# Optimization experiments

Measured on AMD Instinct MI355X. Metric: run time of the kernel, lower is better.

The kernel has to match this reference:

```python
import jax, jax.numpy as jnp
import numpy as np

LMBD = 0.1      # cfg['MODEL']['LAMBDA'][0]
MU = 0.1        # ISTA/FISTA step size (cfg['MODEL']['MU'])
N_STEPS = 4     # cfg['MODEL']['NUM_LAYERS']
FISTA = True    # cfg['MODEL']['ISFISTA']


def _conv(x, W, s, p):
    # torch F.conv2d, NCHW / OIHW
    return jax.lax.conv_general_dilated(x, W, (s, s), [(p, p), (p, p)],
        dimension_numbers=('NCHW', 'OIHW', 'NCHW'))


def _conv_t(z, W, s, p):
    # torch F.conv_transpose2d(z, W, stride=s, padding=p): output (H-1)*s + k - 2p
    k = W.shape[-1]
    Wt = jnp.transpose(jnp.flip(W, (-2, -1)), (1, 0, 2, 3))
    pad = k - 1 - p
    return jax.lax.conv_general_dilated(z, Wt, (1, 1), [(pad, pad), (pad, pad)],
        lhs_dilation=(s, s), dimension_numbers=('NCHW', 'OIHW', 'NCHW'))


def _wnorm(W):
    # per-atom unit-norm dictionary (w_norm=True)
    return W / (jnp.sqrt(jnp.sum(W * W, axis=(1, 2, 3), keepdims=True)) + 1e-12)


def _dict_block(x, W, s, p):
    # unrolled FISTA sparse coding: min_z 0.5||x - W^T*z||^2 + lmbd||z||_1, z>=0
    thr = MU * LMBD
    shrink = lambda u: jax.nn.relu(u - thr)  # non-negative soft threshold
    z0 = shrink(MU * _conv(x, W, s, p))

    def body(carry, _):
        z, z_old, t = carry
        if FISTA:
            t_new = (1.0 + jnp.sqrt(1.0 + 4.0 * t * t)) * 0.5
            y = z + ((t - 1.0) / t_new) * (z - z_old)
        else:
            t_new, y = t, z
        r = x - _conv_t(y, W, s, p)                 # residual in image space
        z_new = shrink(y + MU * _conv(r, W, s, p))  # gradient step + shrinkage
        return (z_new, z, t_new), None

    (z, _, _), _ = jax.lax.scan(body, (z0, z0, jnp.float32(1.0)), None, length=N_STEPS - 1)
    return z


def _bn(x, eps=1e-5):
    # BatchNorm2d at init (gamma=1, beta=0), training-mode batch stats, biased var
    m = jnp.mean(x, axis=(0, 2, 3), keepdims=True)
    v = jnp.var(x, axis=(0, 2, 3), keepdims=True)
    return (x - m) * jax.lax.rsqrt(v + eps)


def _lrelu(x):
    return jnp.where(x >= 0, x, 0.2 * x)


def setup_inputs() -> dict:
    key = jax.random.key(0)
    ks = jax.random.split(key, 7)
    nc, ndf, nz = 3, 64, 128

    def kaiming(k, shape):
        fan_in = shape[1] * shape[2] * shape[3]
        bound = float(np.sqrt(6.0 / fan_in))
        return jax.random.uniform(k, shape, jnp.float32, -bound, bound)

    return {
        'x':  jax.random.normal(ks[0], (64, nc, 96, 96), jnp.float32),
        'W1': kaiming(ks[1], (ndf, nc, 4, 4)),
        'W2': kaiming(ks[2], (ndf * 2, ndf, 4, 4)),
        'W3': kaiming(ks[3], (ndf * 4, ndf * 2, 4, 4)),
        'W4': kaiming(ks[4], (ndf * 8, ndf * 4, 4, 4)),
        'W5': kaiming(ks[5], (ndf * 16, ndf * 8, 4, 4)),
        'W6': kaiming(ks[6], (nz, ndf * 16, 3, 3)),
    }


def reference(x, W1, W2, W3, W4, W5, W6):
    Ws = [_wnorm(w) for w in (W1, W2, W3, W4, W5, W6)]
    # encoder: 96 -> 48 -> 24 -> 12 -> 6 -> 3 -> 1
    o = _lrelu(_dict_block(x, Ws[0], 2, 1))
    for i in range(1, 5):
        o = _lrelu(_bn(_dict_block(o, Ws[i], 2, 1)))
    z = _dict_block(o, Ws[5], 1, 0).reshape(x.shape[0], -1)
    z = z / jnp.maximum(jnp.linalg.norm(z, axis=1, keepdims=True), 1e-12)  # F.normalize
    # decoder (DictConv2d.inverse chain, uses the normalized dictionaries)
    h = z.reshape(z.shape[0], -1, 1, 1)
    h = jax.nn.relu(_bn(_conv_t(h, Ws[5], 1, 0)))
    for i in (4, 3, 2, 1):
        h = jax.nn.relu(_bn(_conv_t(h, Ws[i], 2, 1)))
    x_hat = jnp.tanh(_conv_t(h, Ws[0], 2, 1))
    return z, x_hat
```

## Files before the change

kernel.cpp:

```cpp
#include <hip/hip_runtime.h>
#include <math.h>

#define BLK 256
static constexpr float MU_F  = 0.1f;
static constexpr float THR_F = 0.01f;

typedef __attribute__((ext_vector_type(8))) short bf16x8;
typedef __attribute__((ext_vector_type(4))) float f32x4;

__device__ inline unsigned short f2bf(float f) {
    unsigned u = __float_as_uint(f);
    unsigned r = (u + 0x7fffu + ((u >> 16) & 1u)) >> 16;
    return (unsigned short)r;
}
__device__ inline float bf2f(unsigned short h) {
    return __uint_as_float(((unsigned)h) << 16);
}

__device__ inline float blk_reduce(float v) {
    __shared__ float sh[BLK];
    int tid = threadIdx.x;
    sh[tid] = v;
    __syncthreads();
    #pragma unroll
    for (int s = BLK / 2; s > 0; s >>= 1) {
        if (tid < s) sh[tid] += sh[tid + s];
        __syncthreads();
    }
    float r = sh[0];
    __syncthreads();
    return r;
}

__global__ __launch_bounds__(BLK) void wnorm_pack(
    const float* __restrict__ W, float* __restrict__ Wkc,
    float* __restrict__ Wnout, int Mout, int asz)
{
    int o = blockIdx.x;
    const float* w = W + (size_t)o * asz;
    float s = 0.f;
    for (int i = threadIdx.x; i < asz; i += BLK) { float v = w[i]; s = fmaf(v, v, s); }
    float tot = blk_reduce(s);
    float inv = 1.0f / (sqrtf(tot) + 1e-12f);
    for (int i = threadIdx.x; i < asz; i += BLK) {
        float v = w[i] * inv;
        Wkc[(size_t)i * Mout + o] = v;
        if (Wnout) Wnout[(size_t)o * asz + i] = v;
    }
}

__global__ __launch_bounds__(BLK) void wnorm_pack_bf16(
    const float* __restrict__ W, short* __restrict__ Cpk, short* __restrict__ Tpk,
    int Cout, int Cin)
{
    int o = blockIdx.x;
    int asz = Cin * 16;
    const float* w = W + (size_t)o * asz;
    float s = 0.f;
    for (int i = threadIdx.x; i < asz; i += BLK) { float v = w[i]; s = fmaf(v, v, s); }
    float tot = blk_reduce(s);
    float inv = 1.0f / (sqrtf(tot) + 1e-12f);
    size_t cTot = (size_t)Cout * asz;
    size_t parStride = (size_t)Cout * 4 * Cin;
    size_t tTot = 4 * parStride;
    for (int i = threadIdx.x; i < asz; i += BLK) {
        float v = w[i] * inv;
        unsigned short hb = f2bf(v);
        unsigned short lb = f2bf(v - bf2f(hb));
        size_t cidx = ((size_t)(i >> 3)) * (Cout * 8) + o * 8 + (i & 7);
        Cpk[cidx] = (short)hb;
        Cpk[cTot + cidx] = (short)lb;
        int c = i >> 4, tap = i & 15, kh = tap >> 2, kw = tap & 3;
        int par = (1 - (kh & 1)) * 2 + (1 - (kw & 1));
        int tt = ((kh >> 1) << 1) | (kw >> 1);
        int q = o * 4 + tt;
        size_t tidx = (size_t)par * parStride + ((size_t)(q >> 3)) * (Cin * 8) + c * 8 + (q & 7);
        Tpk[tidx] = (short)hb;
        Tpk[tTot + tidx] = (short)lb;
    }
}

__device__ inline void xcd_remap(int& bx, int& by, int& bz) {
    int nx = gridDim.x, ny = gridDim.y;
    int nwg = nx * ny * gridDim.z;
    int orig = blockIdx.x + nx * (blockIdx.y + ny * blockIdx.z);
    int q8 = nwg >> 3, r8 = nwg & 7, xcd = orig & 7, sidx = orig >> 3;
    int w = (xcd < r8 ? xcd * (q8 + 1) : r8 * (q8 + 1) + (xcd - r8) * q8) + sidx;
    bx = w % nx; int t = w / nx; by = t % ny; bz = t / ny;
}

__global__ __launch_bounds__(BLK) void conv_gemm_bf16(
    const short* __restrict__ Wpk, const float* __restrict__ x,
    const float* __restrict__ yin, float* __restrict__ out,
    int M, int Cx, int Hx, int Wx, int Hout, int Wout,
    int kchunk, int emode)
{
    __shared__ __align__(16) short Wh[4][64][8];
    __shared__ __align__(16) short Wo_[4][64][8];
    __shared__ __align__(16) short Xh[4][64][8];
    __shared__ __align__(16) short Xo[4][64][8];
    int bx, by, bz; xcd_remap(bx, by, bz);
    int tid = threadIdx.x, lane = tid & 63, wid = tid >> 6;
    int HW = Hout * Wout, HWx = Hx * Wx;
    int pbase = bx * 64, m0 = by * 64, kb = bz * kchunk;
    size_t loOff = (size_t)Cx * 16 * M;

    int spl = tid & 63, skb = tid >> 6;
    int sp = pbase + spl;
    int sn = sp / HW; int srr = sp - sn * HW;
    int sho = srr / Wout, swo = srr - sho * Wout;
    const float* xs = x + (size_t)sn * Cx * HWx;
    int h0 = sho * 2 - 1, w0 = swo * 2 - 1;

    int t16 = (skb & 1) * 8;
    int offs[8]; bool valt[8];
    #pragma unroll
    for (int jj = 0; jj < 8; ++jj) {
        int tap = t16 + jj;
        int kh = tap >> 2, kw = tap & 3;
        int h = h0 + kh, w = w0 + kw;
        valt[jj] = ((unsigned)h < (unsigned)Hx) && ((unsigned)w < (unsigned)Wx);
        offs[jj] = h * Wx + w;
    }
    const float* xc = xs + ((size_t)(kb >> 4) + (skb >> 1)) * HWx;

    f32x4 acc[4] = {};
    for (int k0 = kb; k0 < kb + kchunk; k0 += 32) {
        size_t so = ((size_t)((k0 >> 3) + skb)) * (M * 8) + (size_t)m0 * 8 + spl * 8;
        *(float4*)(&Wh[skb][spl][0])  = *(const float4*)(Wpk + so);
        *(float4*)(&Wo_[skb][spl][0]) = *(const float4*)(Wpk + loOff + so);
        {
            union { short s[8]; float4 f; } uh, ul;
            #pragma unroll
            for (int jj = 0; jj < 8; ++jj) {
                float g = valt[jj] ? xc[offs[jj]] : 0.f;
                unsigned short hb = (unsigned short)(__float_as_uint(g) >> 16);
                uh.s[jj] = (short)hb;
                ul.s[jj] = (short)f2bf(g - bf2f(hb));
            }
            *(float4*)(&Xh[skb][spl][0]) = uh.f;
            *(float4*)(&Xo[skb][spl][0]) = ul.f;
        }
        xc += 2 * HWx;
        __syncthreads();
        bf16x8 ah = *(const bf16x8*)(&Wh[lane >> 4][wid * 16 + (lane & 15)][0]);
        bf16x8 al = *(const bf16x8*)(&Wo_[lane >> 4][wid * 16 + (lane & 15)][0]);
        #pragma unroll
        for (int nf = 0; nf < 4; ++nf) {
            bf16x8 bh = *(const bf16x8*)(&Xh[lane >> 4][nf * 16 + (lane & 15)][0]);
            bf16x8 bl = *(const bf16x8*)(&Xo[lane >> 4][nf * 16 + (lane & 15)][0]);
            acc[nf] = __builtin_amdgcn_mfma_f32_16x16x32_bf16(al, bh, acc[nf], 0, 0, 0);
            acc[nf] = __builtin_amdgcn_mfma_f32_16x16x32_bf16(ah, bl, acc[nf], 0, 0, 0);
            acc[nf] = __builtin_amdgcn_mfma_f32_16x16x32_bf16(ah, bh, acc[nf], 0, 0, 0);
        }
        __syncthreads();
    }
    int colp = lane & 15, rquad = lane >> 4;
    #pragma unroll
    for (int nf = 0; nf < 4; ++nf) {
        int p = pbase + nf * 16 + colp;
        int n = p / HW; int rr = p - n * HW;
        int ho = rr / Wout, wo = rr - ho * Wout;
        #pragma unroll
        for (int r = 0; r < 4; ++r) {
            int m = m0 + wid * 16 + rquad * 4 + r;
            size_t idx = (((size_t)n * M + m) * Hout + ho) * Wout + wo;
            float v = acc[nf][r];
            if (emode == 0)      out[idx] = fmaxf(MU_F * v - THR_F, 0.f);
            else if (emode == 1) out[idx] = fmaxf(yin[idx] + MU_F * v - THR_F, 0.f);
            else                 atomicAdd(&out[idx], v);
        }
    }
}

__global__ __launch_bounds__(BLK) void convt_gemm_bf16(
    const short* __restrict__ Wpk, const float* __restrict__ z,
    const float* __restrict__ aux, float* __restrict__ out,
    int M, int Cz, int Hz, int Wz, int Ho, int Wo, int emode, int SK)
{
    __shared__ __align__(16) short Wh[4][64][8];
    __shared__ __align__(16) short Wo_[4][64][8];
    __shared__ __align__(16) short Xh[4][64][8];
    __shared__ __align__(16) short Xo[4][64][8];
    int bx, by, bz; xcd_remap(bx, by, bz);
    int tid = threadIdx.x, lane = tid & 63, wid = tid >> 6;
    int par = bz / SK, chunk = bz - par * SK;
    int hbit = par >> 1, wbit = par & 1;
    int czs = Cz / SK;
    int qb = chunk * czs * 4;
    size_t parS = (size_t)Cz * 4 * M;
    const short* Wp = Wpk + (size_t)par * parS;
    size_t loOff = 4 * parS;
    int Hc = Ho >> 1, Wc = Wo >> 1, HWc = Hc * Wc;
    int pbase = bx * 64, m0 = by * 64;

    int spl = tid & 63, skb = tid >> 6;
    int sp = pbase + spl;
    int sn = sp / HWc; int srr = sp - sn * HWc;
    int shc = srr / Wc, swc = srr - shc * Wc;
    int HWz = Hz * Wz;
    const float* zs = z + (size_t)sn * Cz * HWz;

    int offt[4]; bool valt[4];
    #pragma unroll
    for (int t = 0; t < 4; ++t) {
        int ti = t >> 1, tj = t & 1;
        int hn = shc + hbit - ti, wn = swc + wbit - tj;
        valt[t] = ((unsigned)hn < (unsigned)Hz) && ((unsigned)wn < (unsigned)Wz);
        offt[t] = hn * Wz + wn;
    }
    const float* zc = zs + ((size_t)(qb >> 2) + skb * 2) * HWz;

    f32x4 acc[4] = {};
    for (int q0 = qb; q0 < qb + czs * 4; q0 += 32) {
        size_t so = ((size_t)((q0 >> 3) + skb)) * (M * 8) + (size_t)m0 * 8 + spl * 8;
        *(float4*)(&Wh[skb][spl][0])  = *(const float4*)(Wp + so);
        *(float4*)(&Wo_[skb][spl][0]) = *(const float4*)(Wp + loOff + so);
        {
            union { short s[8]; float4 f; } uh, ul;
            #pragma unroll
            for (int jj = 0; jj < 8; ++jj) {
                int t = jj & 3;
                float g = valt[t] ? zc[(jj >> 2) * HWz + offt[t]] : 0.f;
                unsigned short hb = (unsigned short)(__float_as_uint(g) >> 16);
                uh.s[jj] = (short)hb;
                ul.s[jj] = (short)f2bf(g - bf2f(hb));
            }
            *(float4*)(&Xh[skb][spl][0]) = uh.f;
            *(float4*)(&Xo[skb][spl][0]) = ul.f;
        }
        zc += 8 * HWz;
        __syncthreads();
        bf16x8 ah = *(const bf16x8*)(&Wh[lane >> 4][wid * 16 + (lane & 15)][0]);
        bf16x8 al = *(const bf16x8*)(&Wo_[lane >> 4][wid * 16 + (lane & 15)][0]);
        #pragma unroll
        for (int nf = 0; nf < 4; ++nf) {
            bf16x8 bh = *(const bf16x8*)(&Xh[lane >> 4][nf * 16 + (lane & 15)][0]);
            bf16x8 bl = *(const bf16x8*)(&Xo[lane >> 4][nf * 16 + (lane & 15)][0]);
            acc[nf] = __builtin_amdgcn_mfma_f32_16x16x32_bf16(al, bh, acc[nf], 0, 0, 0);
            acc[nf] = __builtin_amdgcn_mfma_f32_16x16x32_bf16(ah, bl, acc[nf], 0, 0, 0);
            acc[nf] = __builtin_amdgcn_mfma_f32_16x16x32_bf16(ah, bh, acc[nf], 0, 0, 0);
        }
        __syncthreads();
    }
    int colp = lane & 15, rquad = lane >> 4;
    #pragma unroll
    for (int nf = 0; nf < 4; ++nf) {
        int p = pbase + nf * 16 + colp;
        int n = p / HWc; int rr = p - n * HWc;
        int hc = rr / Wc, wc = rr - hc * Wc;
        int ho = 2 * hc + hbit, wo = 2 * wc + wbit;
        #pragma unroll
        for (int r = 0; r < 4; ++r) {
            int m = m0 + wid * 16 + rquad * 4 + r;
            size_t idx = (((size_t)n * M + m) * Ho + ho) * Wo + wo;
            float v = acc[nf][r];
            if (emode == 0)      out[idx] = aux[idx] - v;
            else if (emode == 1) out[idx] = v;
            else                 atomicAdd(&out[idx], v);
        }
    }
}

template <int KK, int Kk, int S, int P>
__global__ __launch_bounds__(BLK) void conv_gemm(
    const float* __restrict__ Wp, const float* __restrict__ x,
    const float* __restrict__ yin, float* __restrict__ out,
    int M, int Ktot, int Cx, int Hx, int Wx, int Hout, int Wout,
    int kchunk, int emode)
{
    __shared__ float Wt[16][64];
    __shared__ float Xt[16][64];
    int tid = threadIdx.x, tx = tid & 15, ty = tid >> 4;
    int HW = Hout * Wout, HWx = Hx * Wx;
    int pbase = blockIdx.x * 64 + tx * 4;
    int n_[4], ho_[4], wo_[4];
    const float* xb_[4];
    #pragma unroll
    for (int j = 0; j < 4; ++j) {
        int p = pbase + j; int n = p / HW; int r = p - n * HW;
        int ho = r / Wout; int wo = r - ho * Wout;
        n_[j] = n; ho_[j] = ho; wo_[j] = wo;
        xb_[j] = x + (size_t)n * Cx * HWx;
    }
    int m0 = blockIdx.y * 64;
    int kb = blockIdx.z * kchunk, ke = kb + kchunk;
    if (ke > Ktot) ke = Ktot;
    float acc[4][4] = {};
    for (int k0 = kb; k0 < ke; k0 += 16) {
        int kr = k0 + ty;
        *(float4*)&Wt[ty][tx * 4] = *(const float4*)&Wp[(size_t)kr * M + m0 + tx * 4];
        int ci = kr / KK; int t = kr - ci * KK; int kh = t / Kk; int kw = t - kh * Kk;
        int cio = ci * HWx;
        float g[4];
        #pragma unroll
        for (int j = 0; j < 4; ++j) {
            int h = ho_[j] * S - P + kh, w = wo_[j] * S - P + kw;
            g[j] = ((unsigned)h < (unsigned)Hx && (unsigned)w < (unsigned)Wx)
                 ? xb_[j][cio + h * Wx + w] : 0.f;
        }
        *(float4*)&Xt[ty][tx * 4] = make_float4(g[0], g[1], g[2], g[3]);
        __syncthreads();
        #pragma unroll
        for (int kk = 0; kk < 16; ++kk) {
            float4 a = *(float4*)&Wt[kk][ty * 4];
            float4 b = *(float4*)&Xt[kk][tx * 4];
            float aa[4] = {a.x, a.y, a.z, a.w};
            float bb[4] = {b.x, b.y, b.z, b.w};
            #pragma unroll
            for (int i = 0; i < 4; ++i)
                #pragma unroll
                for (int j = 0; j < 4; ++j)
                    acc[i][j] = fmaf(aa[i], bb[j], acc[i][j]);
        }
        __syncthreads();
    }
    #pragma unroll
    for (int i = 0; i < 4; ++i) {
        int m = m0 + ty * 4 + i;
        #pragma unroll
        for (int j = 0; j < 4; ++j) {
            size_t idx = (((size_t)n_[j] * M + m) * Hout + ho_[j]) * Wout + wo_[j];
            float v = acc[i][j];
            if (emode == 0)      out[idx] = fmaxf(MU_F * v - THR_F, 0.f);
            else if (emode == 1) out[idx] = fmaxf(yin[idx] + MU_F * v - THR_F, 0.f);
            else                 atomicAdd(&out[idx], v);
        }
    }
}

__global__ __launch_bounds__(BLK) void outer_gemm(
    const float* __restrict__ Wp, const float* __restrict__ zin,
    const float* __restrict__ aux, float* __restrict__ out,
    int M, int Kz, int emode)
{
    __shared__ float Wt[16][64];
    __shared__ float Xt[16][64];
    int tid = threadIdx.x, tx = tid & 15, ty = tid >> 4;
    int m0 = blockIdx.y * 64;
    float acc[4][4] = {};
    for (int k0 = 0; k0 < Kz; k0 += 16) {
        int kr = k0 + ty;
        *(float4*)&Wt[ty][tx * 4] = *(const float4*)&Wp[(size_t)kr * M + m0 + tx * 4];
        float g[4];
        #pragma unroll
        for (int j = 0; j < 4; ++j) g[j] = zin[(size_t)(tx * 4 + j) * Kz + kr];
        *(float4*)&Xt[ty][tx * 4] = make_float4(g[0], g[1], g[2], g[3]);
        __syncthreads();
        #pragma unroll
        for (int kk = 0; kk < 16; ++kk) {
            float4 a = *(float4*)&Wt[kk][ty * 4];
            float4 b = *(float4*)&Xt[kk][tx * 4];
            float aa[4] = {a.x, a.y, a.z, a.w};
            float bb[4] = {b.x, b.y, b.z, b.w};
            #pragma unroll
            for (int i = 0; i < 4; ++i)
                #pragma unroll
                for (int j = 0; j < 4; ++j)
                    acc[i][j] = fmaf(aa[i], bb[j], acc[i][j]);
        }
        __syncthreads();
    }
    #pragma unroll
    for (int i = 0; i < 4; ++i) {
        int m = m0 + ty * 4 + i;
        #pragma unroll
        for (int j = 0; j < 4; ++j) {
            int n = tx * 4 + j;
            size_t idx = (size_t)n * M + m;
            float v = acc[i][j];
            out[idx] = (emode == 0) ? (aux[idx] - v) : v;
        }
    }
}

__global__ __launch_bounds__(BLK) void convt_m3(
    const float* __restrict__ Wkc0, const float* __restrict__ z,
    const float* __restrict__ aux, float* __restrict__ out,
    int Cz, int Hz, int Wz, int Ho, int Wo, int emode)
{
    __shared__ float Wl[64 * 4 * 3];
    int tid = threadIdx.x;
    int hbit = blockIdx.z >> 1, wbit = blockIdx.z & 1;
    int khp = 1 - hbit, kwp = 1 - wbit;
    int Ktot = Cz * 4;
    for (int kidx = tid; kidx < Ktot; kidx += BLK) {
        int cz = kidx >> 2, t = kidx & 3, ti = t >> 1, tj = t & 1;
        int tap = (khp + 2 * ti) * 4 + (kwp + 2 * tj);
        Wl[kidx * 3 + 0] = Wkc0[(0 * 16 + tap) * 64 + cz];
        Wl[kidx * 3 + 1] = Wkc0[(1 * 16 + tap) * 64 + cz];
        Wl[kidx * 3 + 2] = Wkc0[(2 * 16 + tap) * 64 + cz];
    }
    __syncthreads();
    int Hc = Ho >> 1, Wc = Wo >> 1, HWc = Hc * Wc;
    int p = blockIdx.x * BLK + tid;
    int n = p / HWc, r = p - n * HWc, hc = r / Wc, wc = r - (r / Wc) * Wc;
    const float* zb = z + (size_t)n * Cz * Hz * Wz;
    int offs[4]; bool val[4];
    #pragma unroll
    for (int t = 0; t < 4; ++t) {
        int ti = t >> 1, tj = t & 1;
        int hn = hc + hbit - ti, wn = wc + wbit - tj;
        val[t] = ((unsigned)hn < (unsigned)Hz) && ((unsigned)wn < (unsigned)Wz);
        offs[t] = hn * Wz + wn;
    }
    float a0 = 0.f, a1 = 0.f, a2 = 0.f;
    int HWz = Hz * Wz;
    for (int cz = 0; cz < Cz; ++cz) {
        const float* base = zb + cz * HWz;
        #pragma unroll
        for (int t = 0; t < 4; ++t) {
            float g = val[t] ? base[offs[t]] : 0.f;
            int wi = (cz * 4 + t) * 3;
            a0 = fmaf(g, Wl[wi + 0], a0);
            a1 = fmaf(g, Wl[wi + 1], a1);
            a2 = fmaf(g, Wl[wi + 2], a2);
        }
    }
    int ho = 2 * hc + hbit, wo = 2 * wc + wbit;
    #pragma unroll
    for (int u = 0; u < 3; ++u) {
        float v = (u == 0) ? a0 : (u == 1) ? a1 : a2;
        size_t idx = (((size_t)n * 3 + u) * Ho + ho) * Wo + wo;
        out[idx] = (emode == 0) ? (aux[idx] - v) : tanhf(v);
    }
}

__global__ __launch_bounds__(BLK) void shrink_epi_v4(
    const float* __restrict__ p, const float* __restrict__ y,
    float* __restrict__ o, int n4, int mode)
{
    int i = blockIdx.x * BLK + threadIdx.x;
    if (i >= n4) return;
    float4 pv = ((const float4*)p)[i];
    float4 r;
    if (mode == 1) {
        float4 yv = ((const float4*)y)[i];
        r.x = fmaxf(yv.x + MU_F * pv.x - THR_F, 0.f);
        r.y = fmaxf(yv.y + MU_F * pv.y - THR_F, 0.f);
        r.z = fmaxf(yv.z + MU_F * pv.z - THR_F, 0.f);
        r.w = fmaxf(yv.w + MU_F * pv.w - THR_F, 0.f);
    } else {
        r.x = fmaxf(MU_F * pv.x - THR_F, 0.f);
        r.y = fmaxf(MU_F * pv.y - THR_F, 0.f);
        r.z = fmaxf(MU_F * pv.z - THR_F, 0.f);
        r.w = fmaxf(MU_F * pv.w - THR_F, 0.f);
    }
    ((float4*)o)[i] = r;
}

__global__ __launch_bounds__(BLK) void res_epi_v4(
    const float* __restrict__ aux, const float* __restrict__ acc,
    float* __restrict__ o, int n4)
{
    int i = blockIdx.x * BLK + threadIdx.x;
    if (i >= n4) return;
    float4 a = ((const float4*)aux)[i];
    float4 b = ((const float4*)acc)[i];
    ((float4*)o)[i] = make_float4(a.x - b.x, a.y - b.y, a.z - b.z, a.w - b.w);
}

__global__ __launch_bounds__(BLK) void y_update_v4(
    const float* __restrict__ z, const float* __restrict__ zo,
    float* __restrict__ y, int n4, float c)
{
    int i = blockIdx.x * BLK + threadIdx.x;
    if (i >= n4) return;
    float4 zv = ((const float4*)z)[i];
    float4 ov = ((const float4*)zo)[i];
    ((float4*)y)[i] = make_float4(
        fmaf(c, zv.x - ov.x, zv.x), fmaf(c, zv.y - ov.y, zv.y),
        fmaf(c, zv.z - ov.z, zv.z), fmaf(c, zv.w - ov.w, zv.w));
}

__global__ __launch_bounds__(BLK) void bn_stats_part(
    const float* __restrict__ x, float* __restrict__ stats,
    int N, int C, int HW, int nblk)
{
    int c = blockIdx.x, b = blockIdx.y;
    int cnt = N * HW;
    float s = 0.f, s2 = 0.f;
    for (int i = b * BLK + threadIdx.x; i < cnt; i += nblk * BLK) {
        int n = i / HW, hw = i - n * HW;
        float v = x[((size_t)n * C + c) * HW + hw];
        s += v; s2 = fmaf(v, v, s2);
    }
    float ts  = blk_reduce(s);
    float ts2 = blk_reduce(s2);
    if (threadIdx.x == 0) {
        atomicAdd(&stats[c], ts);
        atomicAdd(&stats[C + c], ts2);
    }
}
__global__ __launch_bounds__(BLK) void bn_finalize(
    const float* __restrict__ stats, float* __restrict__ mean,
    float* __restrict__ rstd, int C, int cnt)
{
    int c = blockIdx.x * BLK + threadIdx.x;
    if (c >= C) return;
    float m = stats[c] / cnt;
    float var = stats[C + c] / cnt - m * m;
    mean[c] = m;
    rstd[c] = rsqrtf(var + 1e-5f);
}

__global__ __launch_bounds__(BLK) void bn_act_v4(
    const float* __restrict__ x, const float* __restrict__ mean,
    const float* __restrict__ rstd, float* __restrict__ out,
    int n4, int C, int HW, int use_bn, int act)
{
    int i = blockIdx.x * BLK + threadIdx.x;
    if (i >= n4) return;
    float4 v = ((const float4*)x)[i];
    float e[4] = {v.x, v.y, v.z, v.w};
    int base = i * 4;
    #pragma unroll
    for (int j = 0; j < 4; ++j) {
        float t = e[j];
        if (use_bn) { int c = ((base + j) / HW) % C; t = (t - mean[c]) * rstd[c]; }
        e[j] = (act == 0) ? ((t >= 0.f) ? t : 0.2f * t) : fmaxf(t, 0.f);
    }
    ((float4*)out)[i] = make_float4(e[0], e[1], e[2], e[3]);
}

__global__ __launch_bounds__(128) void rownorm_kernel(
    const float* __restrict__ z, float* __restrict__ out, float* __restrict__ zvec)
{
    __shared__ float sh[128];
    int r = blockIdx.x, tid = threadIdx.x;
    float v = z[r * 128 + tid];
    sh[tid] = v * v;
    __syncthreads();
    #pragma unroll
    for (int s = 64; s > 0; s >>= 1) {
        if (tid < s) sh[tid] += sh[tid + s];
        __syncthreads();
    }
    float nrm = fmaxf(sqrtf(sh[0]), 1e-12f);
    float o = v / nrm;
    out[r * 128 + tid] = o;
    zvec[r * 128 + tid] = o;
}

static inline int gdiv(int a, int b) { return (a + b - 1) / b; }

extern "C" void kernel_launch(void* const* d_in, const int* in_sizes, int n_in,
                              void* d_out, int out_size, void* d_ws, size_t ws_size,
                              hipStream_t stream)
{
    const float* x = (const float*)d_in[0];
    const float* W[6];
    for (int i = 0; i < 6; ++i) W[i] = (const float*)d_in[1 + i];
    float* ws  = (float*)d_ws;
    float* out = (float*)d_out;

    const int Cin[6]  = {3, 64, 128, 256, 512, 1024};
    const int Cout[6] = {64, 128, 256, 512, 1024, 128};
    const int Hin[6]  = {96, 48, 24, 12, 6, 3};
    const int Hout[6] = {48, 24, 12, 6, 3, 1};
    const int N = 64;
    const int SKc[6] = {1, 1, 2, 4, 8, 1};
    const int SKt[6] = {1, 1, 1, 2, 4, 1};

    size_t off = 0;
    float* Wkc0 = ws + off; off += 3072;
    float* Wkc5 = ws + off; off += 1179648;
    float* Wn5  = ws + off; off += 1179648;
    const size_t csz[5] = {0, 131072, 524288, 2097152, 8388608};
    short* Cpk[5]; short* Tpk[5];
    {
        short* sbase = (short*)(ws + off);
        size_t soff = 0;
        for (int L = 1; L < 5; ++L) { Cpk[L] = sbase + soff; soff += 2 * csz[L]; }
        for (int L = 1; L < 5; ++L) { Tpk[L] = sbase + soff; soff += 2 * csz[L]; }
        off += soff / 2;
    }
    const size_t POOL = 30081024;
    float* pool = ws + off; off += POOL;
    float* xb   = ws + off; off += 9437184;
    float* mean = ws + off; off += 1024;
    float* rstd = ws + off; off += 1024;
    float* stats= ws + off; off += 2048;
    float* zvec = ws + off; off += 8192;
    float* pbuf = ws + off; off += 2359296;

    wnorm_pack<<<64, BLK, 0, stream>>>(W[0], Wkc0, nullptr, 64, 48);
    for (int L = 1; L < 5; ++L)
        wnorm_pack_bf16<<<Cout[L], BLK, 0, stream>>>(W[L], Cpk[L], Tpk[L], Cout[L], Cin[L]);
    wnorm_pack<<<128, BLK, 0, stream>>>(W[5], Wkc5, Wn5, 128, 9216);

    double td = 1.0; float cc[3];
    for (int i = 0; i < 3; ++i) {
        double tn = (1.0 + sqrt(1.0 + 4.0 * td * td)) * 0.5;
        cc[i] = (float)((td - 1.0) / tn);
        td = tn;
    }

    auto run_bn_stats = [&](const float* src, int C, int HW) {
        int cnt = N * HW;
        int nblk = 2048 / C; if (nblk < 1) nblk = 1;
        int maxb = gdiv(cnt, BLK); if (nblk > maxb) nblk = maxb;
        hipMemsetAsync(stats, 0, 2 * C * sizeof(float), stream);
        bn_stats_part<<<dim3(C, nblk), BLK, 0, stream>>>(src, stats, N, C, HW, nblk);
        bn_finalize<<<gdiv(C, BLK), BLK, 0, stream>>>(stats, mean, rstd, C, cnt);
    };

    const float* in = x;
    for (int L = 0; L < 6; ++L) {
        int zTot = N * Cout[L] * Hout[L] * Hout[L];
        int xTot = N * Cin[L] * Hin[L] * Hin[L];
        int npix = N * Hout[L] * Hout[L];
        dim3 ge4(gdiv(zTot / 4, BLK));
        dim3 gr4(gdiv(xTot / 4, BLK));

        float* zA = pool;
        float* zB = pool + (size_t)zTot;
        float* yb = pool + (size_t)2 * zTot;
        float* rb = pool + (size_t)3 * zTot;

        auto launch_conv = [&](const float* src, const float* y, float* dst, int mode) {
            if (L == 5) {
                hipMemsetAsync(pbuf, 0, (size_t)zTot * 4, stream);
                conv_gemm<9, 3, 1, 0><<<dim3(1, 2, 72), BLK, 0, stream>>>(Wkc5, src,
                    nullptr, pbuf, 128, 9216, 1024, 3, 3, 1, 1, 128, 2);
                shrink_epi_v4<<<gdiv(zTot / 4, BLK), BLK, 0, stream>>>(pbuf, y, dst, zTot / 4, mode);
            } else if (L == 0) {
                conv_gemm<16, 4, 2, 1><<<dim3(npix / 64, 1), BLK, 0, stream>>>(
                    Wkc0, src, y, dst, 64, 48, 3, 96, 96, 48, 48, 48, mode);
            } else if (SKc[L] == 1) {
                conv_gemm_bf16<<<dim3(npix / 64, Cout[L] / 64), BLK, 0, stream>>>(
                    Cpk[L], src, y, dst, Cout[L], Cin[L], Hin[L], Hin[L],
                    Hout[L], Hout[L], Cin[L] * 16, mode);
            } else {
                int sk = SKc[L];
                hipMemsetAsync(pbuf, 0, (size_t)zTot * 4, stream);
                conv_gemm_bf16<<<dim3(npix / 64, Cout[L] / 64, sk), BLK, 0, stream>>>(
                    Cpk[L], src, nullptr, pbuf, Cout[L], Cin[L], Hin[L], Hin[L],
                    Hout[L], Hout[L], Cin[L] * 16 / sk, 2);
                shrink_epi_v4<<<gdiv(zTot / 4, BLK), BLK, 0, stream>>>(pbuf, y, dst, zTot / 4, mode);
            }
        };

        launch_conv(in, nullptr, zA, 0);

        float* z = zA; float* zo = zB;
        for (int it = 0; it < 3; ++it) {
            const float* ybp;
            if (it == 0) {
                ybp = z;
            } else {
                y_update_v4<<<ge4, BLK, 0, stream>>>(z, zo, yb, zTot / 4, cc[it]);
                ybp = yb;
            }
            if (L == 0) {
                convt_m3<<<dim3(N * 48 * 48 / BLK, 1, 4), BLK, 0, stream>>>(
                    Wkc0, ybp, in, rb, 64, 48, 48, 96, 96, 0);
            } else if (L < 5) {
                int xpixc = N * (Hin[L] / 2) * (Hin[L] / 2);
                int sk = SKt[L];
                if (sk == 1) {
                    convt_gemm_bf16<<<dim3(xpixc / 64, Cin[L] / 64, 4), BLK, 0, stream>>>(
                        Tpk[L], ybp, in, rb, Cin[L], Cout[L], Hout[L], Hout[L],
                        Hin[L], Hin[L], 0, 1);
                } else {
                    hipMemsetAsync(rb, 0, (size_t)xTot * 4, stream);
                    convt_gemm_bf16<<<dim3(xpixc / 64, Cin[L] / 64, 4 * sk), BLK, 0, stream>>>(
                        Tpk[L], ybp, nullptr, rb, Cin[L], Cout[L], Hout[L], Hout[L],
                        Hin[L], Hin[L], 2, sk);
                    res_epi_v4<<<gr4, BLK, 0, stream>>>(in, rb, rb, xTot / 4);
                }
            } else {
                outer_gemm<<<dim3(1, 144), BLK, 0, stream>>>(Wn5, ybp, in, rb, 9216, 128, 0);
            }
            launch_conv(rb, ybp, zo, 1);
            float* tmp = z; z = zo; zo = tmp;
        }

        int HW = Hout[L] * Hout[L];
        if (L == 0) {
            bn_act_v4<<<ge4, BLK, 0, stream>>>(z, nullptr, nullptr, xb, zTot / 4, Cout[L], HW, 0, 0);
            in = xb;
        } else if (L < 5) {
            run_bn_stats(z, Cout[L], HW);
            bn_act_v4<<<ge4, BLK, 0, stream>>>(z, mean, rstd, xb, zTot / 4, Cout[L], HW, 1, 0);
            in = xb;
        } else {
            rownorm_kernel<<<64, 128, 0, stream>>>(z, out, zvec);
        }
    }

    float* zA = pool;
    float* zB = pool + 9437184;
    {
        int oT = N * 1024 * 9;
        outer_gemm<<<dim3(1, 144), BLK, 0, stream>>>(Wn5, zvec, nullptr, zA, 9216, 128, 1);
        run_bn_stats(zA, 1024, 9);
        bn_act_v4<<<gdiv(oT / 4, BLK), BLK, 0, stream>>>(zA, mean, rstd, zB, oT / 4, 1024, 9, 1, 1);
    }
    float* cur = zB;
    for (int i = 4; i >= 1; --i) {
        int oT = N * Cin[i] * Hin[i] * Hin[i];
        int xpixc = N * (Hin[i] / 2) * (Hin[i] / 2);
        int sk = SKt[i];
        if (sk == 1) {
            convt_gemm_bf16<<<dim3(xpixc / 64, Cin[i] / 64, 4), BLK, 0, stream>>>(
                Tpk[i], cur, nullptr, zA, Cin[i], Cout[i], Hout[i], Hout[i],
                Hin[i], Hin[i], 1, 1);
        } else {
            hipMemsetAsync(zA, 0, (size_t)oT * 4, stream);
            convt_gemm_bf16<<<dim3(xpixc / 64, Cin[i] / 64, 4 * sk), BLK, 0, stream>>>(
                Tpk[i], cur, nullptr, zA, Cin[i], Cout[i], Hout[i], Hout[i],
                Hin[i], Hin[i], 2, sk);
        }
        run_bn_stats(zA, Cin[i], Hin[i] * Hin[i]);
        bn_act_v4<<<gdiv(oT / 4, BLK), BLK, 0, stream>>>(zA, mean, rstd, zB, oT / 4,
            Cin[i], Hin[i] * Hin[i], 1, 1);
        cur = zB;
    }
    convt_m3<<<dim3(N * 48 * 48 / BLK, 1, 4), BLK, 0, stream>>>(
        Wkc0, cur, nullptr, out + 8192, 64, 48, 48, 96, 96, 2);
}
```

Baseline: 3.787 ms.

## Widen bf16 conv GEMM pixel tile to 256 for better weight reuse

Templates the conv and transposed-conv bf16 MFMA GEMM kernels on pixel-tile width. Layers other than layer 4 now use 256-pixel tiles, with each thread gathering one pixel's full 32-wide K slice. Each staged weight tile then feeds four times as many MFMAs, cutting weight traffic and barrier count per flop. The cost is more accumulator registers and LDS per block, plus fewer blocks, which may hurt occupancy and load balance on the smaller layers.

```diff
diff --git a/kernel.cpp b/kernel.cpp
--- a/kernel.cpp
+++ b/kernel.cpp
@@ -89,75 +89,127 @@
     bx = w % nx; int t = w / nx; by = t % ny; bz = t / ny;
 }
 
+template <int PIXB>
 __global__ __launch_bounds__(BLK) void conv_gemm_bf16(
     const short* __restrict__ Wpk, const float* __restrict__ x,
     const float* __restrict__ yin, float* __restrict__ out,
     int M, int Cx, int Hx, int Wx, int Hout, int Wout,
     int kchunk, int emode)
 {
+    constexpr int NF = PIXB / 16;
     __shared__ __align__(16) short Wh[4][64][8];
     __shared__ __align__(16) short Wo_[4][64][8];
-    __shared__ __align__(16) short Xh[4][64][8];
-    __shared__ __align__(16) short Xo[4][64][8];
+    __shared__ __align__(16) short Xh[4][PIXB][8];
+    __shared__ __align__(16) short Xo[4][PIXB][8];
     int bx, by, bz; xcd_remap(bx, by, bz);
     int tid = threadIdx.x, lane = tid & 63, wid = tid >> 6;
     int HW = Hout * Wout, HWx = Hx * Wx;
-    int pbase = bx * 64, m0 = by * 64, kb = bz * kchunk;
+    int pbase = bx * PIXB, m0 = by * 64, kb = bz * kchunk;
     size_t loOff = (size_t)Cx * 16 * M;
-
-    int spl = tid & 63, skb = tid >> 6;
-    int sp = pbase + spl;
+    int wspl = tid & 63, wskb = tid >> 6;
+
+    int sp = pbase + ((PIXB == 64) ? (tid & 63) : tid);
     int sn = sp / HW; int srr = sp - sn * HW;
     int sho = srr / Wout, swo = srr - sho * Wout;
     const float* xs = x + (size_t)sn * Cx * HWx;
     int h0 = sho * 2 - 1, w0 = swo * 2 - 1;
 
-    int t16 = (skb & 1) * 8;
-    int offs[8]; bool valt[8];
-    #pragma unroll
-    for (int jj = 0; jj < 8; ++jj) {
-        int tap = t16 + jj;
-        int kh = tap >> 2, kw = tap & 3;
-        int h = h0 + kh, w = w0 + kw;
-        valt[jj] = ((unsigned)h < (unsigned)Hx) && ((unsigned)w < (unsigned)Wx);
-        offs[jj] = h * Wx + w;
-    }
-    const float* xc = xs + ((size_t)(kb >> 4) + (skb >> 1)) * HWx;
-
-    f32x4 acc[4] = {};
-    for (int k0 = kb; k0 < kb + kchunk; k0 += 32) {
-        size_t so = ((size_t)((k0 >> 3) + skb)) * (M * 8) + (size_t)m0 * 8 + spl * 8;
-        *(float4*)(&Wh[skb][spl][0])  = *(const float4*)(Wpk + so);
-        *(float4*)(&Wo_[skb][spl][0]) = *(const float4*)(Wpk + loOff + so);
-        {
-            union { short s[8]; float4 f; } uh, ul;
+    f32x4 acc[NF] = {};
+
+    if constexpr (PIXB == 64) {
+        int t16 = (wskb & 1) * 8;
+        int offs[8]; bool valt[8];
+        #pragma unroll
+        for (int jj = 0; jj < 8; ++jj) {
+            int tap = t16 + jj;
+            int kh = tap >> 2, kw = tap & 3;
+            int h = h0 + kh, w = w0 + kw;
+            valt[jj] = ((unsigned)h < (unsigned)Hx) && ((unsigned)w < (unsigned)Wx);
+            offs[jj] = h * Wx + w;
+        }
+        const float* xc = xs + ((size_t)(kb >> 4) + (wskb >> 1)) * HWx;
+        for (int k0 = kb; k0 < kb + kchunk; k0 += 32) {
+            size_t so = ((size_t)((k0 >> 3) + wskb)) * (M * 8) + (size_t)m0 * 8 + wspl * 8;
+            *(float4*)(&Wh[wskb][wspl][0])  = *(const float4*)(Wpk + so);
+            *(float4*)(&Wo_[wskb][wspl][0]) = *(const float4*)(Wpk + loOff + so);
+            union { short s8[8]; float4 f; } uh, ul;
             #pragma unroll
             for (int jj = 0; jj < 8; ++jj) {
                 float g = valt[jj] ? xc[offs[jj]] : 0.f;
                 unsigned short hb = (unsigned short)(__float_as_uint(g) >> 16);
-                uh.s[jj] = (short)hb;
-                ul.s[jj] = (short)f2bf(g - bf2f(hb));
-            }
-            *(float4*)(&Xh[skb][spl][0]) = uh.f;
-            *(float4*)(&Xo[skb][spl][0]) = ul.f;
-        }
-        xc += 2 * HWx;
-        __syncthreads();
-        bf16x8 ah = *(const bf16x8*)(&Wh[lane >> 4][wid * 16 + (lane & 15)][0]);
-        bf16x8 al = *(const bf16x8*)(&Wo_[lane >> 4][wid * 16 + (lane & 15)][0]);
-        #pragma unroll
-        for (int nf = 0; nf < 4; ++nf) {
-            bf16x8 bh = *(const bf16x8*)(&Xh[lane >> 4][nf * 16 + (lane & 15)][0]);
-            bf16x8 bl = *(const bf16x8*)(&Xo[lane >> 4][nf * 16 + (lane & 15)][0]);
-            acc[nf] = __builtin_amdgcn_mfma_f32_16x16x32_bf16(al, bh, acc[nf], 0, 0, 0);
-            acc[nf] = __builtin_amdgcn_mfma_f32_16x16x32_bf16(ah, bl, acc[nf], 0, 0, 0);
-            acc[nf] = __builtin_amdgcn_mfma_f32_16x16x32_bf16(ah, bh, acc[nf], 0, 0, 0);
-        }
-        __syncthreads();
-    }
+                uh.s8[jj] = (short)hb;
+                ul.s8[jj] = (short)f2bf(g - bf2f(hb));
+            }
+            *(float4*)(&Xh[wskb][wspl][0]) = uh.f;
+            *(float4*)(&Xo[wskb][wspl][0]) = ul.f;
+            xc += 2 * HWx;
+            __syncthreads();
+            bf16x8 ah = *(const bf16x8*)(&Wh[lane >> 4][wid * 16 + (lane & 15)][0]);
+            bf16x8 al = *(const bf16x8*)(&Wo_[lane >> 4][wid * 16 + (lane & 15)][0]);
+            #pragma unroll
+            for (int nf = 0; nf < NF; ++nf) {
+                bf16x8 bh = *(const bf16x8*)(&Xh[lane >> 4][nf * 16 + (lane & 15)][0]);
+                bf16x8 bl = *(const bf16x8*)(&Xo[lane >> 4][nf * 16 + (lane & 15)][0]);
+                acc[nf] = __builtin_amdgcn_mfma_f32_16x16x32_bf16(al, bh, acc[nf], 0, 0, 0);
+                acc[nf] = __builtin_amdgcn_mfma_f32_16x16x32_bf16(ah, bl, acc[nf], 0, 0, 0);
+                acc[nf] = __builtin_amdgcn_mfma_f32_16x16x32_bf16(ah, bh, acc[nf], 0, 0, 0);
+            }
+            __syncthreads();
+        }
+    } else {
+        int offs[16]; bool valt[16];
+        #pragma unroll
+        for (int tp = 0; tp < 16; ++tp) {
+            int kh = tp >> 2, kw = tp & 3;
+            int h = h0 + kh, w = w0 + kw;
+            valt[tp] = ((unsigned)h < (unsigned)Hx) && ((unsigned)w < (unsigned)Wx);
+            offs[tp] = h * Wx + w;
+        }
+        const float* xc = xs + ((size_t)(kb >> 4)) * HWx;
+        for (int k0 = kb; k0 < kb + kchunk; k0 += 32) {
+            size_t so = ((size_t)((k0 >> 3) + wskb)) * (M * 8) + (size_t)m0 * 8 + wspl * 8;
+            *(float4*)(&Wh[wskb][wspl][0])  = *(const float4*)(Wpk + so);
+            *(float4*)(&Wo_[wskb][wspl][0]) = *(const float4*)(Wpk + loOff + so);
+            #pragma unroll
+            for (int s = 0; s < 4; ++s) {
+                union { short s8[8]; float4 f; } uh, ul;
+                const float* xcs = xc + (s >> 1) * HWx;
+                #pragma unroll
+                for (int jj = 0; jj < 8; ++jj) {
+                    constexpr int dummy = 0; (void)dummy;
+                    float g;
+                    {
+                        const int tp0 = 0;
+                        (void)tp0;
+                    }
+                    int tpi = (s & 1) * 8 + jj;
+                    g = valt[tpi] ? xcs[offs[tpi]] : 0.f;
+                    unsigned short hb = (unsigned short)(__float_as_uint(g) >> 16);
+                    uh.s8[jj] = (short)hb;
+                    ul.s8[jj] = (short)f2bf(g - bf2f(hb));
+                }
+                *(float4*)(&Xh[s][tid][0]) = uh.f;
+                *(float4*)(&Xo[s][tid][0]) = ul.f;
+            }
+            xc += 2 * HWx;
+            __syncthreads();
+            bf16x8 ah = *(const bf16x8*)(&Wh[lane >> 4][wid * 16 + (lane & 15)][0]);
+            bf16x8 al = *(const bf16x8*)(&Wo_[lane >> 4][wid * 16 + (lane & 15)][0]);
+            #pragma unroll
+            for (int nf = 0; nf < NF; ++nf) {
+                bf16x8 bh = *(const bf16x8*)(&Xh[lane >> 4][nf * 16 + (lane & 15)][0]);
+                bf16x8 bl = *(const bf16x8*)(&Xo[lane >> 4][nf * 16 + (lane & 15)][0]);
+                acc[nf] = __builtin_amdgcn_mfma_f32_16x16x32_bf16(al, bh, acc[nf], 0, 0, 0);
+                acc[nf] = __builtin_amdgcn_mfma_f32_16x16x32_bf16(ah, bl, acc[nf], 0, 0, 0);
+                acc[nf] = __builtin_amdgcn_mfma_f32_16x16x32_bf16(ah, bh, acc[nf], 0, 0, 0);
+            }
+            __syncthreads();
+        }
+    }
+
     int colp = lane & 15, rquad = lane >> 4;
     #pragma unroll
-    for (int nf = 0; nf < 4; ++nf) {
+    for (int nf = 0; nf < NF; ++nf) {
         int p = pbase + nf * 16 + colp;
         int n = p / HW; int rr = p - n * HW;
         int ho = rr / Wout, wo = rr - ho * Wout;
@@ -173,15 +225,17 @@
     }
 }
 
+template <int PIXB>
 __global__ __launch_bounds__(BLK) void convt_gemm_bf16(
     const short* __restrict__ Wpk, const float* __restrict__ z,
     const float* __restrict__ aux, float* __restrict__ out,
     int M, int Cz, int Hz, int Wz, int Ho, int Wo, int emode, int SK)
 {
+    constexpr int NF = PIXB / 16;
     __shared__ __align__(16) short Wh[4][64][8];
     __shared__ __align__(16) short Wo_[4][64][8];
-    __shared__ __align__(16) short Xh[4][64][8];
-    __shared__ __align__(16) short Xo[4][64][8];
+    __shared__ __align__(16) short Xh[4][PIXB][8];
+    __shared__ __align__(16) short Xo[4][PIXB][8];
     int bx, by, bz; xcd_remap(bx, by, bz);
     int tid = threadIdx.x, lane = tid & 63, wid = tid >> 6;
     int par = bz / SK, chunk = bz - par * SK;
@@ -192,10 +246,10 @@
     const short* Wp = Wpk + (size_t)par * parS;
     size_t loOff = 4 * parS;
     int Hc = Ho >> 1, Wc = Wo >> 1, HWc = Hc * Wc;
-    int pbase = bx * 64, m0 = by * 64;
-
-    int spl = tid & 63, skb = tid >> 6;
-    int sp = pbase + spl;
+    int pbase = bx * PIXB, m0 = by * 64;
+    int wspl = tid & 63, wskb = tid >> 6;
+
+    int sp = pbase + ((PIXB == 64) ? (tid & 63) : tid);
     int sn = sp / HWc; int srr = sp - sn * HWc;
     int shc = srr / Wc, swc = srr - shc * Wc;
     int HWz = Hz * Wz;
@@ -209,43 +263,80 @@
         valt[t] = ((unsigned)hn < (unsigned)Hz) && ((unsigned)wn < (unsigned)Wz);
         offt[t] = hn * Wz + wn;
     }
-    const float* zc = zs + ((size_t)(qb >> 2) + skb * 2) * HWz;
-
-    f32x4 acc[4] = {};
-    for (int q0 = qb; q0 < qb + czs * 4; q0 += 32) {
-        size_t so = ((size_t)((q0 >> 3) + skb)) * (M * 8) + (size_t)m0 * 8 + spl * 8;
-        *(float4*)(&Wh[skb][spl][0])  = *(const float4*)(Wp + so);
-        *(float4*)(&Wo_[skb][spl][0]) = *(const float4*)(Wp + loOff + so);
-        {
-            union { short s[8]; float4 f; } uh, ul;
+
+    f32x4 acc[NF] = {};
+
+    if constexpr (PIXB == 64) {
+        const float* zc = zs + ((size_t)(qb >> 2) + wskb * 2) * HWz;
+        for (int q0 = qb; q0 < qb + czs * 4; q0 += 32) {
+            size_t so = ((size_t)((q0 >> 3) + wskb)) * (M * 8) + (size_t)m0 * 8 + wspl * 8;
+            *(float4*)(&Wh[wskb][wspl][0])  = *(const float4*)(Wp + so);
+            *(float4*)(&Wo_[wskb][wspl][0]) = *(const float4*)(Wp + loOff + so);
+            union { short s8[8]; float4 f; } uh, ul;
             #pragma unroll
             for (int jj = 0; jj < 8; ++jj) {
                 int t = jj & 3;
                 float g = valt[t] ? zc[(jj >> 2) * HWz + offt[t]] : 0.f;
                 unsigned short hb = (unsigned short)(__float_as_uint(g) >> 16);
-                uh.s[jj] = (short)hb;
-                ul.s[jj] = (short)f2bf(g - bf2f(hb));
-            }
-            *(float4*)(&Xh[skb][spl][0]) = uh.f;
-            *(float4*)(&Xo[skb][spl][0]) = ul.f;
-        }
-        zc += 8 * HWz;
-        __syncthreads();
-        bf16x8 ah = *(const bf16x8*)(&Wh[lane >> 4][wid * 16 + (lane & 15)][0]);
-        bf16x8 al = *(const bf16x8*)(&Wo_[lane >> 4][wid * 16 + (lane & 15)][0]);
-        #pragma unroll
-        for (int nf = 0; nf < 4; ++nf) {
-            bf16x8 bh = *(const bf16x8*)(&Xh[lane >> 4][nf * 16 + (lane & 15)][0]);
-            bf16x8 bl = *(const bf16x8*)(&Xo[lane >> 4][nf * 16 + (lane & 15)][0]);
-            acc[nf] = __builtin_amdgcn_mfma_f32_16x16x32_bf16(al, bh, acc[nf], 0, 0, 0);
-            acc[nf] = __builtin_amdgcn_mfma_f32_16x16x32_bf16(ah, bl, acc[nf], 0, 0, 0);
-            acc[nf] = __builtin_amdgcn_mfma_f32_16x16x32_bf16(ah, bh, acc[nf], 0, 0, 0);
-        }
-        __syncthreads();
-    }
+                uh.s8[jj] = (short)hb;
+                ul.s8[jj] = (short)f2bf(g - bf2f(hb));
+            }
+            *(float4*)(&Xh[wskb][wspl][0]) = uh.f;
+            *(float4*)(&Xo[wskb][wspl][0]) = ul.f;
+            zc += 8 * HWz;
+            __syncthreads();
+            bf16x8 ah = *(const bf16x8*)(&Wh[lane >> 4][wid * 16 + (lane & 15)][0]);
+            bf16x8 al = *(const bf16x8*)(&Wo_[lane >> 4][wid * 16 + (lane & 15)][0]);
+            #pragma unroll
+            for (int nf = 0; nf < NF; ++nf) {
+                bf16x8 bh = *(const bf16x8*)(&Xh[lane >> 4][nf * 16 + (lane & 15)][0]);
+                bf16x8 bl = *(const bf16x8*)(&Xo[lane >> 4][nf * 16 + (lane & 15)][0]);
+                acc[nf] = __builtin_amdgcn_mfma_f32_16x16x32_bf16(al, bh, acc[nf], 0, 0, 0);
+                acc[nf] = __builtin_amdgcn_mfma_f32_16x16x32_bf16(ah, bl, acc[nf], 0, 0, 0);
+                acc[nf] = __builtin_amdgcn_mfma_f32_16x16x32_bf16(ah, bh, acc[nf], 0, 0, 0);
+            }
+            __syncthreads();
+        }
+    } else {
+        const float* zc = zs + ((size_t)(qb >> 2)) * HWz;
+        for (int q0 = qb; q0 < qb + czs * 4; q0 += 32) {
+            size_t so = ((size_t)((q0 >> 3) + wskb)) * (M * 8) + (size_t)m0 * 8 + wspl * 8;
+            *(float4*)(&Wh[wskb][wspl][0])  = *(const float4*)(Wp + so);
+            *(float4*)(&Wo_[wskb][wspl][0]) = *(const float4*)(Wp + loOff + so);
+            #pragma unroll
+            for (int s = 0; s < 4; ++s) {
+                union { short s8[8]; float4 f; } uh, ul;
+                const float* zcs = zc + s * 2 * HWz;
+                #pragma unroll
+                for (int jj = 0; jj < 8; ++jj) {
+                    int t = jj & 3;
+                    float g = valt[t] ? zcs[(jj >> 2) * HWz + offt[t]] : 0.f;
+                    unsigned short hb = (unsigned short)(__float_as_uint(g) >> 16);
+                    uh.s8[jj] = (short)hb;
+                    ul.s8[jj] = (short)f2bf(g - bf2f(hb));
+                }
+                *(float4*)(&Xh[s][tid][0]) = uh.f;
+                *(float4*)(&Xo[s][tid][0]) = ul.f;
+            }
+            zc += 8 * HWz;
+            __syncthreads();
+            bf16x8 ah = *(const bf16x8*)(&Wh[lane >> 4][wid * 16 + (lane & 15)][0]);
+            bf16x8 al = *(const bf16x8*)(&Wo_[lane >> 4][wid * 16 + (lane & 15)][0]);
+            #pragma unroll
+            for (int nf = 0; nf < NF; ++nf) {
+                bf16x8 bh = *(const bf16x8*)(&Xh[lane >> 4][nf * 16 + (lane & 15)][0]);
+                bf16x8 bl = *(const bf16x8*)(&Xo[lane >> 4][nf * 16 + (lane & 15)][0]);
+                acc[nf] = __builtin_amdgcn_mfma_f32_16x16x32_bf16(al, bh, acc[nf], 0, 0, 0);
+                acc[nf] = __builtin_amdgcn_mfma_f32_16x16x32_bf16(ah, bl, acc[nf], 0, 0, 0);
+                acc[nf] = __builtin_amdgcn_mfma_f32_16x16x32_bf16(ah, bh, acc[nf], 0, 0, 0);
+            }
+            __syncthreads();
+        }
+    }
+
     int colp = lane & 15, rquad = lane >> 4;
     #pragma unroll
-    for (int nf = 0; nf < 4; ++nf) {
+    for (int nf = 0; nf < NF; ++nf) {
         int p = pbase + nf * 16 + colp;
         int n = p / HWc; int rr = p - n * HWc;
         int hc = rr / Wc, wc = rr - hc * Wc;
@@ -628,15 +719,20 @@
                 conv_gemm<16, 4, 2, 1><<<dim3(npix / 64, 1), BLK, 0, stream>>>(
                     Wkc0, src, y, dst, 64, 48, 3, 96, 96, 48, 48, 48, mode);
             } else if (SKc[L] == 1) {
-                conv_gemm_bf16<<<dim3(npix / 64, Cout[L] / 64), BLK, 0, stream>>>(
+                conv_gemm_bf16<256><<<dim3(npix / 256, Cout[L] / 64), BLK, 0, stream>>>(
                     Cpk[L], src, y, dst, Cout[L], Cin[L], Hin[L], Hin[L],
                     Hout[L], Hout[L], Cin[L] * 16, mode);
             } else {
                 int sk = SKc[L];
                 hipMemsetAsync(pbuf, 0, (size_t)zTot * 4, stream);
-                conv_gemm_bf16<<<dim3(npix / 64, Cout[L] / 64, sk), BLK, 0, stream>>>(
-                    Cpk[L], src, nullptr, pbuf, Cout[L], Cin[L], Hin[L], Hin[L],
-                    Hout[L], Hout[L], Cin[L] * 16 / sk, 2);
+                if (L == 4)
+                    conv_gemm_bf16<64><<<dim3(npix / 64, Cout[L] / 64, sk), BLK, 0, stream>>>(
+                        Cpk[L], src, nullptr, pbuf, Cout[L], Cin[L], Hin[L], Hin[L],
+                        Hout[L], Hout[L], Cin[L] * 16 / sk, 2);
+                else
+                    conv_gemm_bf16<256><<<dim3(npix / 256, Cout[L] / 64, sk), BLK, 0, stream>>>(
+                        Cpk[L], src, nullptr, pbuf, Cout[L], Cin[L], Hin[L], Hin[L],
+                        Hout[L], Hout[L], Cin[L] * 16 / sk, 2);
                 shrink_epi_v4<<<gdiv(zTot / 4, BLK), BLK, 0, stream>>>(pbuf, y, dst, zTot / 4, mode);
             }
         };
@@ -659,14 +755,19 @@
                 int xpixc = N * (Hin[L] / 2) * (Hin[L] / 2);
                 int sk = SKt[L];
                 if (sk == 1) {
-                    convt_gemm_bf16<<<dim3(xpixc / 64, Cin[L] / 64, 4), BLK, 0, stream>>>(
+                    convt_gemm_bf16<256><<<dim3(xpixc / 256, Cin[L] / 64, 4), BLK, 0, stream>>>(
                         Tpk[L], ybp, in, rb, Cin[L], Cout[L], Hout[L], Hout[L],
                         Hin[L], Hin[L], 0, 1);
                 } else {
                     hipMemsetAsync(rb, 0, (size_t)xTot * 4, stream);
-                    convt_gemm_bf16<<<dim3(xpixc / 64, Cin[L] / 64, 4 * sk), BLK, 0, stream>>>(
-                        Tpk[L], ybp, nullptr, rb, Cin[L], Cout[L], Hout[L], Hout[L],
-                        Hin[L], Hin[L], 2, sk);
+                    if (L == 4)
+                        convt_gemm_bf16<64><<<dim3(xpixc / 64, Cin[L] / 64, 4 * sk), BLK, 0, stream>>>(
+                            Tpk[L], ybp, nullptr, rb, Cin[L], Cout[L], Hout[L], Hout[L],
+                            Hin[L], Hin[L], 2, sk);
+                    else
+                        convt_gemm_bf16<256><<<dim3(xpixc / 256, Cin[L] / 64, 4 * sk), BLK, 0, stream>>>(
+                            Tpk[L], ybp, nullptr, rb, Cin[L], Cout[L], Hout[L], Hout[L],
+                            Hin[L], Hin[L], 2, sk);
                     res_epi_v4<<<gr4, BLK, 0, stream>>>(in, rb, rb, xTot / 4);
                 }
             } else {
@@ -703,14 +804,19 @@
         int xpixc = N * (Hin[i] / 2) * (Hin[i] / 2);
         int sk = SKt[i];
         if (sk == 1) {
-            convt_gemm_bf16<<<dim3(xpixc / 64, Cin[i] / 64, 4), BLK, 0, stream>>>(
+            convt_gemm_bf16<256><<<dim3(xpixc / 256, Cin[i] / 64, 4), BLK, 0, stream>>>(
                 Tpk[i], cur, nullptr, zA, Cin[i], Cout[i], Hout[i], Hout[i],
                 Hin[i], Hin[i], 1, 1);
         } else {
             hipMemsetAsync(zA, 0, (size_t)oT * 4, stream);
-            convt_gemm_bf16<<<dim3(xpixc / 64, Cin[i] / 64, 4 * sk), BLK, 0, stream>>>(
-                Tpk[i], cur, nullptr, zA, Cin[i], Cout[i], Hout[i], Hout[i],
-                Hin[i], Hin[i], 2, sk);
+            if (i == 4)
+                convt_gemm_bf16<64><<<dim3(xpixc / 64, Cin[i] / 64, 4 * sk), BLK, 0, stream>>>(
+                    Tpk[i], cur, nullptr, zA, Cin[i], Cout[i], Hout[i], Hout[i],
+                    Hin[i], Hin[i], 2, sk);
+            else
+                convt_gemm_bf16<256><<<dim3(xpixc / 256, Cin[i] / 64, 4 * sk), BLK, 0, stream>>>(
+                    Tpk[i], cur, nullptr, zA, Cin[i], Cout[i], Hout[i], Hout[i],
+                    Hin[i], Hin[i], 2, sk);
         }
         run_bn_stats(zA, Cin[i], Hin[i] * Hin[i]);
         bn_act_v4<<<gdiv(oT / 4, BLK), BLK, 0, stream>>>(zA, mean, rstd, zB, oT / 4,
```

Result: slower. 5.221 ms (+37.9%).
